# Kernel optimization log

Hardware: AMD Instinct MI355X
Metric: run time of the kernel (lower is better)

The kernel has to match this reference:

```python
import jax, jax.numpy as jnp
import numpy as np

B = 4096          # number of instance groups (images)
C = 81            # num_classes + 1 (fixed by the 81x81 prior_rel buffer)
D_K = 64
MAX_N = 128       # max instances per group


def setup_inputs() -> dict:
    key = jax.random.key(0)
    rng = np.random.default_rng(0)
    ni = rng.integers(1, MAX_N + 1, size=B)
    ni[0] = MAX_N  # pin the max so padded length is deterministic
    num_instances = jnp.asarray(ni, dtype=jnp.int32)
    total = int(ni.sum())
    ks = jax.random.split(key, 10)
    s_in = 1.0 / np.sqrt(C)
    s_dk = 1.0 / np.sqrt(D_K)
    return {
        'x': jax.random.normal(ks[0], (total, C), jnp.float32),
        'num_instances': num_instances,
        'prior_rel': jax.random.normal(ks[1], (C, C), jnp.float32) * s_in,
        'wq': jax.random.normal(ks[2], (C, D_K), jnp.float32) * s_in,
        'bq': jnp.zeros((D_K,), jnp.float32),
        'wk': jax.random.normal(ks[3], (C, D_K), jnp.float32) * s_in,
        'bk': jnp.zeros((D_K,), jnp.float32),
        'wv': jax.random.normal(ks[4], (C, D_K), jnp.float32) * s_in,
        'bv': jnp.zeros((D_K,), jnp.float32),
        'wu': jax.random.normal(ks[5], (D_K, C), jnp.float32) * s_dk,
        'bu': jnp.zeros((C,), jnp.float32),
    }


def reference(x, num_instances, prior_rel, wq, bq, wk, bk, wv, bv, wu, bu):
    # num_instances is static ragged metadata (the torch code keeps it as a
    # Python list), so it is safe to pull concrete ints from it here.
    ni = np.asarray(num_instances)
    Bn = ni.shape[0]
    M = int(ni.max())
    total = x.shape[0]

    counts = jnp.asarray(ni, jnp.int32)                      # [B]
    offsets = jnp.concatenate([jnp.zeros((1,), jnp.int32),
                               jnp.cumsum(counts)[:-1]])      # [B]
    pos = jnp.arange(M, dtype=jnp.int32)                      # [M]
    mask = pos[None, :] < counts[:, None]                     # [B, M] valid slots
    idx = offsets[:, None] + pos[None, :]                     # [B, M] flat gather idx
    idx_safe = jnp.where(mask, idx, 0)

    # pad: split x into ragged groups, zero-pad each to length M
    padded = x[idx_safe] * mask[:, :, None].astype(x.dtype)   # [B, M, C]

    q = padded @ wq + bq                                      # [B, M, d_k]
    k = padded @ wk + bk                                      # [B, M, d_k]
    v = (padded @ prior_rel) @ wv + bv                        # [B, M, d_k]

    scores = jnp.einsum('bmd,bnd->bmn', q, k) / jnp.sqrt(
        jnp.asarray(D_K, x.dtype))                            # [B, M, M]
    # mask padded KEY columns (queries on padded rows are dropped at unpad)
    scores = jnp.where(mask[:, None, :], scores, -jnp.inf)
    probs = jax.nn.softmax(scores, axis=2)
    out = jnp.einsum('bmn,bnd->bmd', probs, v)                # [B, M, d_k]
    out = out @ wu + bu                                       # [B, M, C]

    # unpad: scatter valid rows back to their ragged flat positions
    tgt = jnp.where(mask, idx, total)                         # dump pad rows past end
    flat = jnp.zeros((total + 1, out.shape[-1]), out.dtype)
    flat = flat.at[tgt.reshape(-1)].set(out.reshape(-1, out.shape[-1]))
    return flat[:total]
```

## Files before the change

### kernel.cpp

```cpp
#include <hip/hip_runtime.h>
#include <hip/hip_bf16.h>


typedef __attribute__((ext_vector_type(8))) short short8;
typedef __attribute__((ext_vector_type(4))) float f32x4;
typedef __attribute__((ext_vector_type(4))) short short4v;

constexpr int C  = 81;
constexpr int DK = 64;
constexpr int CP = 96;

constexpr int OFF_K  = 0;
constexpr int OFF_VT = 128 * 64;
constexpr int SMEM_TOT = OFF_VT + 64 * 128;

__device__ inline int kidx(int row, int colu) {
    return OFF_K + row * 64 + (colu ^ ((row & 7) << 3));
}
__device__ inline int vidx(int dim, int colu) {
    return OFF_VT + dim * 128 + (colu ^ ((dim & 15) << 3));
}

__device__ inline ushort f2b(float f) {
    __hip_bfloat16 h = __float2bfloat16(f);
    return *reinterpret_cast<ushort*>(&h);
}
__device__ inline uint pack2bf(float a, float b) {
    return (uint)f2b(a) | ((uint)f2b(b) << 16);
}
__device__ inline uint shflu(uint v, int srcLane) {
    return (uint)__shfl((int)v, srcLane, 64);
}
union U8 { short8 s; uint u[4]; };

__device__ inline short8 cvt8(const f32x4 u0, const f32x4 u1) {
    short8 a;
    #pragma unroll
    for (int e = 0; e < 4; e++) {
        a[e]     = (short)f2b(u0[e]);
        a[e + 4] = (short)f2b(u1[e]);
    }
    return a;
}

__device__ inline void loadx(const float* __restrict__ xr, int quad, f32x4* u) {
    const int c0 = quad * 8;
    __builtin_memcpy(&u[0], xr + c0, 16);
    __builtin_memcpy(&u[1], xr + c0 + 4, 16);
    __builtin_memcpy(&u[2], xr + 32 + c0, 16);
    __builtin_memcpy(&u[3], xr + 32 + c0 + 4, 16);
    u[4] = f32x4{0.f, 0.f, 0.f, 0.f};
    u[5] = f32x4{0.f, 0.f, 0.f, 0.f};
    if (quad < 2) {
        __builtin_memcpy(&u[4], xr + 64 + c0, 16);
        __builtin_memcpy(&u[5], xr + 64 + c0 + 4, 16);
    } else if (quad == 2) {
        u[4][0] = xr[80];
    }
}

#define MFMA16(a, b, c) __builtin_amdgcn_mfma_f32_16x16x32_bf16((a), (b), (c), 0, 0, 0)

__global__ void scan_counts(const int* __restrict__ counts,
                            uint* __restrict__ meta, int n) {
    __shared__ int part[256];
    __shared__ int hist[129];
    __shared__ int start[130];
    const int tid = threadIdx.x;
    for (int i = tid; i < 129; i += 256) hist[i] = 0;
    __syncthreads();
    const int per = (n + 255) >> 8;
    const int base = tid * per;
    int s = 0;
    for (int i = 0; i < per; i++) {
        const int idx = base + i;
        if (idx < n) {
            int c = counts[idx];
            if (c < 0) c = 0; if (c > 128) c = 128;
            s += counts[idx];
            atomicAdd(&hist[c], 1);
        }
    }
    part[tid] = s;
    __syncthreads();
    for (int off = 1; off < 256; off <<= 1) {
        const int v = (tid >= off) ? part[tid - off] : 0;
        __syncthreads();
        part[tid] += v;
        __syncthreads();
    }
    if (tid == 0) {
        start[128] = 0;
        for (int c = 127; c >= 0; c--) start[c] = start[c + 1] + hist[c + 1];
    }
    __syncthreads();
    int run = (tid == 0) ? 0 : part[tid - 1];
    for (int i = 0; i < per; i++) {
        const int idx = base + i;
        if (idx < n) {
            int c = counts[idx];
            int cc = c; if (cc < 0) cc = 0; if (cc > 128) cc = 128;
            const int pos = atomicAdd(&start[cc], 1);
            meta[pos] = (uint)run | ((uint)c << 24);
            run += c;
        }
    }
}

__global__ void prep_weights(const float* __restrict__ prior,
                             const float* __restrict__ wq, const float* __restrict__ wk,
                             const float* __restrict__ wv, const float* __restrict__ wu,
                             ushort* __restrict__ wqT, ushort* __restrict__ wkT,
                             ushort* __restrict__ wvT, ushort* __restrict__ wuT) {
    int idx = blockIdx.x * 256 + threadIdx.x;
    int sec = idx / (DK * CP);
    int i   = idx - sec * (DK * CP);
    if (sec == 0 || sec == 1) {
        int n = i / CP, k = i - (i / CP) * CP;
        const float* w = (sec == 0) ? wq : wk;
        ushort* dst    = (sec == 0) ? wqT : wkT;
        dst[n * CP + k] = (k < C) ? f2b(w[k * DK + n]) : (ushort)0;
    } else if (sec == 2) {
        int n = i / CP, k = i - (i / CP) * CP;
        float s = 0.f;
        if (k < C)
            for (int e = 0; e < C; e++) s = fmaf(prior[k * C + e], wv[e * DK + n], s);
        wvT[n * CP + k] = (k < C) ? f2b(s) : (ushort)0;
    } else {
        int n = i / DK, k = i - (i / DK) * DK;
        wuT[n * DK + k] = (n < C) ? f2b(wu[k * C + n]) : (ushort)0;
    }
}

__launch_bounds__(256, 4)
__global__ void ravnet_mfma(const float* __restrict__ x,
                            const uint* __restrict__ meta,
                            const ushort* __restrict__ wqT, const ushort* __restrict__ wkT,
                            const ushort* __restrict__ wvT, const ushort* __restrict__ wuT,
                            const float* __restrict__ bq, const float* __restrict__ bk,
                            const float* __restrict__ bv, const float* __restrict__ bu,
                            float* __restrict__ out) {
    __shared__ __align__(16) ushort sm[SMEM_TOT];

    const uint mw  = meta[blockIdx.x];
    const int  N   = (int)(mw >> 24);
    const long off = (long)(mw & 0xFFFFFFu);
    const int tid  = threadIdx.x;
    const int lane = tid & 63;
    const int wave = tid >> 6;
    const int quad = lane >> 4;
    const int m16  = lane & 15;
    const int NT8  = (N + 15) >> 4;
    const int NT4  = (N + 31) >> 5;
    const float* xsrc = x + off * C;

    const int srcE = ((quad & 1) << 5) + m16;
    const int srcO = srcE + 16;
    const bool hi  = (quad >> 1) != 0;

    short8 aq[2][2];

    const bool a0 = wave < NT8;
    const bool a1 = (wave + 4) < NT8;
    if (a0) {
        f32x4 xu0[6], xu1[6];
        {
            const int row = wave * 16 + m16;
            const float* xr = xsrc + (long)((row < N) ? row : (N - 1)) * C;
            loadx(xr, quad, xu0);
        }
        if (a1) {
            const int row = (wave + 4) * 16 + m16;
            const float* xr = xsrc + (long)((row < N) ? row : (N - 1)) * C;
            loadx(xr, quad, xu1);
        }
        short8 ax2[2][3];
        ax2[0][0] = cvt8(xu0[0], xu0[1]);
        ax2[0][1] = cvt8(xu0[2], xu0[3]);
        ax2[0][2] = cvt8(xu0[4], xu0[5]);
        if (a1) {
            ax2[1][0] = cvt8(xu1[0], xu1[1]);
            ax2[1][1] = cvt8(xu1[2], xu1[3]);
            ax2[1][2] = cvt8(xu1[4], xu1[5]);
        }
        uint qpk[2][4][2];
        #pragma unroll
        for (int nt = 0; nt < 4; nt++) {
            const ushort* wp = wqT + (nt * 16 + m16) * CP + quad * 8;
            const short8 f0 = *(const short8*)(wp);
            const short8 f1 = *(const short8*)(wp + 32);
            const short8 f2 = *(const short8*)(wp + 64);
            const f32x4 b4 = *(const f32x4*)(bq + nt * 16 + quad * 4);
            {
                f32x4 acc = {0.f, 0.f, 0.f, 0.f};
                acc = MFMA16(f0, ax2[0][0], acc);
                acc = MFMA16(f1, ax2[0][1], acc);
                acc = MFMA16(f2, ax2[0][2], acc);
                qpk[0][nt][0] = pack2bf(acc[0] + b4[0], acc[1] + b4[1]);
                qpk[0][nt][1] = pack2bf(acc[2] + b4[2], acc[3] + b4[3]);
            }
            if (a1) {
                f32x4 acc = {0.f, 0.f, 0.f, 0.f};
                acc = MFMA16(f0, ax2[1][0], acc);
                acc = MFMA16(f1, ax2[1][1], acc);
                acc = MFMA16(f2, ax2[1][2], acc);
                qpk[1][nt][0] = pack2bf(acc[0] + b4[0], acc[1] + b4[1]);
                qpk[1][nt][1] = pack2bf(acc[2] + b4[2], acc[3] + b4[3]);
            }
        }
        #pragma unroll
        for (int t = 0; t < 2; t++) {
            if (t == 0 || a1) {
                #pragma unroll
                for (int ks = 0; ks < 2; ks++) {
                    uint a0v = shflu(qpk[t][2 * ks][0], srcE), b0v = shflu(qpk[t][2 * ks + 1][0], srcE);
                    uint a1v = shflu(qpk[t][2 * ks][1], srcE), b1v = shflu(qpk[t][2 * ks + 1][1], srcE);
                    uint a2v = shflu(qpk[t][2 * ks][0], srcO), b2v = shflu(qpk[t][2 * ks + 1][0], srcO);
                    uint a3v = shflu(qpk[t][2 * ks][1], srcO), b3v = shflu(qpk[t][2 * ks + 1][1], srcO);
                    U8 u;
                    u.u[0] = hi ? b0v : a0v;  u.u[1] = hi ? b1v : a1v;
                    u.u[2] = hi ? b2v : a2v;  u.u[3] = hi ? b3v : a3v;
                    aq[t][ks] = u.s;
                }
            }
        }
        #pragma unroll
        for (int nt = 0; nt < 4; nt++) {
            const ushort* wp = wkT + (nt * 16 + m16) * CP + quad * 8;
            const short8 f0 = *(const short8*)(wp);
            const short8 f1 = *(const short8*)(wp + 32);
            const short8 f2 = *(const short8*)(wp + 64);
            const f32x4 b4 = *(const f32x4*)(bk + nt * 16 + quad * 4);
            {
                f32x4 acc = {0.f, 0.f, 0.f, 0.f};
                acc = MFMA16(f0, ax2[0][0], acc);
                acc = MFMA16(f1, ax2[0][1], acc);
                acc = MFMA16(f2, ax2[0][2], acc);
                short4v pk4;
                #pragma unroll
                for (int r = 0; r < 4; r++) pk4[r] = (short)f2b(acc[r] + b4[r]);
                *(short4v*)(sm + kidx(wave * 16 + m16, nt * 16 + quad * 4)) = pk4;
            }
            if (a1) {
                f32x4 acc = {0.f, 0.f, 0.f, 0.f};
                acc = MFMA16(f0, ax2[1][0], acc);
                acc = MFMA16(f1, ax2[1][1], acc);
                acc = MFMA16(f2, ax2[1][2], acc);
                short4v pk4;
                #pragma unroll
                for (int r = 0; r < 4; r++) pk4[r] = (short)f2b(acc[r] + b4[r]);
                *(short4v*)(sm + kidx((wave + 4) * 16 + m16, nt * 16 + quad * 4)) = pk4;
            }
        }
        #pragma unroll
        for (int nt = 0; nt < 4; nt++) {
            const ushort* wp = wvT + (nt * 16 + m16) * CP + quad * 8;
            const short8 f0 = *(const short8*)(wp);
            const short8 f1 = *(const short8*)(wp + 32);
            const short8 f2 = *(const short8*)(wp + 64);
            const float bb = bv[nt * 16 + m16];
            {
                f32x4 acc = {0.f, 0.f, 0.f, 0.f};
                acc = MFMA16(ax2[0][0], f0, acc);
                acc = MFMA16(ax2[0][1], f1, acc);
                acc = MFMA16(ax2[0][2], f2, acc);
                short4v pk4;
                #pragma unroll
                for (int r = 0; r < 4; r++) pk4[r] = (short)f2b(acc[r] + bb);
                *(short4v*)(sm + vidx(nt * 16 + m16, wave * 16 + quad * 4)) = pk4;
            }
            if (a1) {
                f32x4 acc = {0.f, 0.f, 0.f, 0.f};
                acc = MFMA16(ax2[1][0], f0, acc);
                acc = MFMA16(ax2[1][1], f1, acc);
                acc = MFMA16(ax2[1][2], f2, acc);
                short4v pk4;
                #pragma unroll
                for (int r = 0; r < 4; r++) pk4[r] = (short)f2b(acc[r] + bb);
                *(short4v*)(sm + vidx(nt * 16 + m16, (wave + 4) * 16 + quad * 4)) = pk4;
            }
        }
    }
    if (NT8 & 1) {
        const int R = NT8 * 16;
        const int d = tid >> 2, c4 = (tid & 3) << 2;
        short4v z = {0, 0, 0, 0};
        *(short4v*)(sm + vidx(d, R + c4)) = z;
    }
    __syncthreads();

    constexpr float SCALE = 0.18033688011112042f;
    #pragma unroll
    for (int t = 0; t < 2; t++) {
        const int qt = wave + 4 * t;
        if (qt < NT8) {
            f32x4 sacc[8];
            #pragma unroll
            for (int ct = 0; ct < 8; ct++) {
                if (ct < NT8) {
                    f32x4 a = {0.f, 0.f, 0.f, 0.f};
                    #pragma unroll
                    for (int ks = 0; ks < 2; ks++) {
                        short8 kb = *(const short8*)(sm + kidx(ct * 16 + m16, ks * 32 + quad * 8));
                        a = MFMA16(kb, aq[t][ks], a);
                    }
                    sacc[ct] = a;
                }
            }
            float lr = 0.f;
            #pragma unroll
            for (int ct = 0; ct < 8; ct++) if (ct < NT8) {
                #pragma unroll
                for (int r = 0; r < 4; r++) {
                    const bool valid = (ct * 16 + quad * 4 + r) < N;
                    float p = valid ? __builtin_exp2f(sacc[ct][r] * SCALE) : 0.f;
                    sacc[ct][r] = p;
                    lr += p;
                }
            }
            lr += __shfl_xor(lr, 16, 64);
            lr += __shfl_xor(lr, 32, 64);
            const float linv = 1.f / lr;
            uint pk[8][2];
            #pragma unroll
            for (int ct = 0; ct < 8; ct++) {
                if (ct < NT8) {
                    pk[ct][0] = pack2bf(sacc[ct][0], sacc[ct][1]);
                    pk[ct][1] = pack2bf(sacc[ct][2], sacc[ct][3]);
                } else {
                    pk[ct][0] = 0u; pk[ct][1] = 0u;
                }
            }
            short8 ap[4];
            #pragma unroll
            for (int kt = 0; kt < 4; kt++) {
                if (kt < NT4) {
                    uint a0v = shflu(pk[2 * kt][0], srcE), b0v = shflu(pk[2 * kt + 1][0], srcE);
                    uint a1v = shflu(pk[2 * kt][1], srcE), b1v = shflu(pk[2 * kt + 1][1], srcE);
                    uint a2v = shflu(pk[2 * kt][0], srcO), b2v = shflu(pk[2 * kt + 1][0], srcO);
                    uint a3v = shflu(pk[2 * kt][1], srcO), b3v = shflu(pk[2 * kt + 1][1], srcO);
                    U8 u;
                    u.u[0] = hi ? b0v : a0v;  u.u[1] = hi ? b1v : a1v;
                    u.u[2] = hi ? b2v : a2v;  u.u[3] = hi ? b3v : a3v;
                    ap[kt] = u.s;
                }
            }
            uint opk[4][2];
            #pragma unroll
            for (int ot = 0; ot < 4; ot++) {
                f32x4 oa = {0.f, 0.f, 0.f, 0.f};
                #pragma unroll
                for (int kt = 0; kt < 4; kt++) if (kt < NT4) {
                    short8 vb = *(const short8*)(sm + vidx(ot * 16 + m16, kt * 32 + quad * 8));
                    oa = MFMA16(vb, ap[kt], oa);
                }
                opk[ot][0] = pack2bf(oa[0] * linv, oa[1] * linv);
                opk[ot][1] = pack2bf(oa[2] * linv, oa[3] * linv);
            }
            short8 ao[2];
            #pragma unroll
            for (int ks = 0; ks < 2; ks++) {
                uint a0v = shflu(opk[2 * ks][0], srcE), b0v = shflu(opk[2 * ks + 1][0], srcE);
                uint a1v = shflu(opk[2 * ks][1], srcE), b1v = shflu(opk[2 * ks + 1][1], srcE);
                uint a2v = shflu(opk[2 * ks][0], srcO), b2v = shflu(opk[2 * ks + 1][0], srcO);
                uint a3v = shflu(opk[2 * ks][1], srcO), b3v = shflu(opk[2 * ks + 1][1], srcO);
                U8 u;
                u.u[0] = hi ? b0v : a0v;  u.u[1] = hi ? b1v : a1v;
                u.u[2] = hi ? b2v : a2v;  u.u[3] = hi ? b3v : a3v;
                ao[ks] = u.s;
            }
            const int xrow = qt * 16 + m16;
            float* orow = out + (off + xrow) * C;
            #pragma unroll
            for (int ct = 0; ct < 6; ct++) {
                f32x4 acc = {0.f, 0.f, 0.f, 0.f};
                #pragma unroll
                for (int ks = 0; ks < 2; ks++) {
                    short8 wb = *(const short8*)(wuT + (ct * 16 + m16) * DK + ks * 32 + quad * 8);
                    acc = MFMA16(wb, ao[ks], acc);
                }
                const int e0 = ct * 16 + quad * 4;
                if (xrow < N) {
                    if (e0 + 3 < C) {
                        const f32x4 b4 = *(const f32x4*)(bu + e0);
                        acc[0] += b4[0]; acc[1] += b4[1];
                        acc[2] += b4[2]; acc[3] += b4[3];
                        __builtin_memcpy(orow + e0, &acc, 16);
                    } else if (e0 == 80) {
                        orow[80] = acc[0] + bu[80];
                    }
                }
            }
        }
    }
}

extern "C" void kernel_launch(void* const* d_in, const int* in_sizes, int n_in,
                              void* d_out, int out_size, void* d_ws, size_t ws_size,
                              hipStream_t stream) {
    const float* x      = (const float*)d_in[0];
    const int*   counts = (const int*)  d_in[1];
    const float* prior  = (const float*)d_in[2];
    const float* wq     = (const float*)d_in[3];
    const float* bq     = (const float*)d_in[4];
    const float* wk     = (const float*)d_in[5];
    const float* bk     = (const float*)d_in[6];
    const float* wv     = (const float*)d_in[7];
    const float* bv     = (const float*)d_in[8];
    const float* wu     = (const float*)d_in[9];
    const float* bu     = (const float*)d_in[10];
    float* out = (float*)d_out;

    const int B = in_sizes[1];

    uint*   meta = (uint*)d_ws;
    ushort* wqT = (ushort*)((char*)d_ws + (((size_t)B * sizeof(uint) + 255) & ~(size_t)255));
    ushort* wkT = wqT + DK * CP;
    ushort* wvT = wkT + DK * CP;
    ushort* wuT = wvT + DK * CP;

    scan_counts<<<1, 256, 0, stream>>>(counts, meta, B);
    prep_weights<<<(4 * DK * CP + 255) / 256, 256, 0, stream>>>(
        prior, wq, wk, wv, wu, wqT, wkT, wvT, wuT);
    ravnet_mfma<<<B, 256, 0, stream>>>(x, meta,
                                       wqT, wkT, wvT, wuT,
                                       bq, bk, bv, bu, out);
}
```

Baseline: 243.5 us.

## Process both query tiles of a wave jointly to share K/V LDS loads

The attention phase now handles a wave's two query tiles together through a templated lambda (dual or single path). Each K and V fragment read from shared memory, and each Wu weight load, feeds two MFMAs instead of being reloaded per tile, and the independent MFMA chains can interleave. The x row loads for both tiles are also issued up front to overlap their global memory latency. In exchange the dual path roughly doubles live accumulator and packing registers, which could lower occupancy or cause spills, and two code paths are compiled.

```diff
diff --git a/kernel.cpp b/kernel.cpp
--- a/kernel.cpp
+++ b/kernel.cpp
@@ -32,6 +32,12 @@
     return (uint)__shfl((int)v, srcLane, 64);
 }
 union U8 { short8 s; uint u[4]; };
+
+__device__ __forceinline__ f32x4 ld4u(const float* p) {
+    f32x4 v;
+    __builtin_memcpy(&v, p, 16);
+    return v;
+}
 
 __device__ inline short8 cvt8(const f32x4 u0, const f32x4 u1) {
     short8 a;
@@ -43,23 +49,20 @@
     return a;
 }
 
-__device__ inline void loadx(const float* __restrict__ xr, int quad, f32x4* u) {
-    const int c0 = quad * 8;
-    __builtin_memcpy(&u[0], xr + c0, 16);
-    __builtin_memcpy(&u[1], xr + c0 + 4, 16);
-    __builtin_memcpy(&u[2], xr + 32 + c0, 16);
-    __builtin_memcpy(&u[3], xr + 32 + c0 + 4, 16);
-    u[4] = f32x4{0.f, 0.f, 0.f, 0.f};
-    u[5] = f32x4{0.f, 0.f, 0.f, 0.f};
-    if (quad < 2) {
-        __builtin_memcpy(&u[4], xr + 64 + c0, 16);
-        __builtin_memcpy(&u[5], xr + 64 + c0 + 4, 16);
-    } else if (quad == 2) {
-        u[4][0] = xr[80];
-    }
-}
-
 #define MFMA16(a, b, c) __builtin_amdgcn_mfma_f32_16x16x32_bf16((a), (b), (c), 0, 0, 0)
+
+#define XPOSE(dst, pA0, pA1, pB0, pB1) do {                                   \
+    uint _a0 = shflu(pA0, srcE), _b0 = shflu(pB0, srcE);                      \
+    uint _a1 = shflu(pA1, srcE), _b1 = shflu(pB1, srcE);                      \
+    uint _a2 = shflu(pA0, srcO), _b2 = shflu(pB0, srcO);                      \
+    uint _a3 = shflu(pA1, srcO), _b3 = shflu(pB1, srcO);                      \
+    U8 _u;                                                                    \
+    _u.u[0] = hi ? _b0 : _a0;  _u.u[1] = hi ? _b1 : _a1;                      \
+    _u.u[2] = hi ? _b2 : _a2;  _u.u[3] = hi ? _b3 : _a3;                      \
+    dst = _u.s; } while (0)
+
+struct BT { static constexpr bool value = true;  };
+struct BF { static constexpr bool value = false; };
 
 __global__ void scan_counts(const int* __restrict__ counts,
                             uint* __restrict__ meta, int n) {
@@ -163,25 +166,32 @@
     const bool a0 = wave < NT8;
     const bool a1 = (wave + 4) < NT8;
     if (a0) {
-        f32x4 xu0[6], xu1[6];
-        {
-            const int row = wave * 16 + m16;
-            const float* xr = xsrc + (long)((row < N) ? row : (N - 1)) * C;
-            loadx(xr, quad, xu0);
-        }
+        const int c0 = quad * 8;
+        const int row0 = wave * 16 + m16;
+        const int row1 = (wave + 4) * 16 + m16;
+        const float* xr0 = xsrc + (long)((row0 < N) ? row0 : (N - 1)) * C;
+        const float* xr1 = a1 ? (xsrc + (long)((row1 < N) ? row1 : (N - 1)) * C) : xr0;
+        f32x4 p00 = ld4u(xr0 + c0),      p01 = ld4u(xr0 + c0 + 4);
+        f32x4 p02 = ld4u(xr0 + 32 + c0), p03 = ld4u(xr0 + 32 + c0 + 4);
+        f32x4 p10 = ld4u(xr1 + c0),      p11 = ld4u(xr1 + c0 + 4);
+        f32x4 p12 = ld4u(xr1 + 32 + c0), p13 = ld4u(xr1 + 32 + c0 + 4);
+        f32x4 p04 = {0.f, 0.f, 0.f, 0.f}, p05 = {0.f, 0.f, 0.f, 0.f};
+        f32x4 p14 = {0.f, 0.f, 0.f, 0.f}, p15 = {0.f, 0.f, 0.f, 0.f};
+        if (quad < 2) {
+            p04 = ld4u(xr0 + 64 + c0); p05 = ld4u(xr0 + 64 + c0 + 4);
+            p14 = ld4u(xr1 + 64 + c0); p15 = ld4u(xr1 + 64 + c0 + 4);
+        } else if (quad == 2) {
+            p04[0] = xr0[80];
+            p14[0] = xr1[80];
+        }
+        short8 ax2[2][3];
+        ax2[0][0] = cvt8(p00, p01);
+        ax2[0][1] = cvt8(p02, p03);
+        ax2[0][2] = cvt8(p04, p05);
         if (a1) {
-            const int row = (wave + 4) * 16 + m16;
-            const float* xr = xsrc + (long)((row < N) ? row : (N - 1)) * C;
-            loadx(xr, quad, xu1);
-        }
-        short8 ax2[2][3];
-        ax2[0][0] = cvt8(xu0[0], xu0[1]);
-        ax2[0][1] = cvt8(xu0[2], xu0[3]);
-        ax2[0][2] = cvt8(xu0[4], xu0[5]);
-        if (a1) {
-            ax2[1][0] = cvt8(xu1[0], xu1[1]);
-            ax2[1][1] = cvt8(xu1[2], xu1[3]);
-            ax2[1][2] = cvt8(xu1[4], xu1[5]);
+            ax2[1][0] = cvt8(p10, p11);
+            ax2[1][1] = cvt8(p12, p13);
+            ax2[1][2] = cvt8(p14, p15);
         }
         uint qpk[2][4][2];
         #pragma unroll
@@ -209,20 +219,14 @@
             }
         }
         #pragma unroll
-        for (int t = 0; t < 2; t++) {
-            if (t == 0 || a1) {
-                #pragma unroll
-                for (int ks = 0; ks < 2; ks++) {
-                    uint a0v = shflu(qpk[t][2 * ks][0], srcE), b0v = shflu(qpk[t][2 * ks + 1][0], srcE);
-                    uint a1v = shflu(qpk[t][2 * ks][1], srcE), b1v = shflu(qpk[t][2 * ks + 1][1], srcE);
-                    uint a2v = shflu(qpk[t][2 * ks][0], srcO), b2v = shflu(qpk[t][2 * ks + 1][0], srcO);
-                    uint a3v = shflu(qpk[t][2 * ks][1], srcO), b3v = shflu(qpk[t][2 * ks + 1][1], srcO);
-                    U8 u;
-                    u.u[0] = hi ? b0v : a0v;  u.u[1] = hi ? b1v : a1v;
-                    u.u[2] = hi ? b2v : a2v;  u.u[3] = hi ? b3v : a3v;
-                    aq[t][ks] = u.s;
-                }
-            }
+        for (int ks = 0; ks < 2; ks++)
+            XPOSE(aq[0][ks], qpk[0][2 * ks][0], qpk[0][2 * ks][1],
+                             qpk[0][2 * ks + 1][0], qpk[0][2 * ks + 1][1]);
+        if (a1) {
+            #pragma unroll
+            for (int ks = 0; ks < 2; ks++)
+                XPOSE(aq[1][ks], qpk[1][2 * ks][0], qpk[1][2 * ks][1],
+                                 qpk[1][2 * ks + 1][0], qpk[1][2 * ks + 1][1]);
         }
         #pragma unroll
         for (int nt = 0; nt < 4; nt++) {
@@ -290,108 +294,131 @@
     __syncthreads();
 
     constexpr float SCALE = 0.18033688011112042f;
-    #pragma unroll
-    for (int t = 0; t < 2; t++) {
-        const int qt = wave + 4 * t;
-        if (qt < NT8) {
-            f32x4 sacc[8];
-            #pragma unroll
-            for (int ct = 0; ct < 8; ct++) {
-                if (ct < NT8) {
-                    f32x4 a = {0.f, 0.f, 0.f, 0.f};
-                    #pragma unroll
-                    for (int ks = 0; ks < 2; ks++) {
-                        short8 kb = *(const short8*)(sm + kidx(ct * 16 + m16, ks * 32 + quad * 8));
-                        a = MFMA16(kb, aq[t][ks], a);
-                    }
-                    sacc[ct] = a;
-                }
-            }
-            float lr = 0.f;
-            #pragma unroll
-            for (int ct = 0; ct < 8; ct++) if (ct < NT8) {
-                #pragma unroll
-                for (int r = 0; r < 4; r++) {
-                    const bool valid = (ct * 16 + quad * 4 + r) < N;
-                    float p = valid ? __builtin_exp2f(sacc[ct][r] * SCALE) : 0.f;
-                    sacc[ct][r] = p;
-                    lr += p;
-                }
-            }
-            lr += __shfl_xor(lr, 16, 64);
-            lr += __shfl_xor(lr, 32, 64);
-            const float linv = 1.f / lr;
-            uint pk[8][2];
-            #pragma unroll
-            for (int ct = 0; ct < 8; ct++) {
-                if (ct < NT8) {
-                    pk[ct][0] = pack2bf(sacc[ct][0], sacc[ct][1]);
-                    pk[ct][1] = pack2bf(sacc[ct][2], sacc[ct][3]);
-                } else {
-                    pk[ct][0] = 0u; pk[ct][1] = 0u;
-                }
-            }
-            short8 ap[4];
-            #pragma unroll
-            for (int kt = 0; kt < 4; kt++) {
-                if (kt < NT4) {
-                    uint a0v = shflu(pk[2 * kt][0], srcE), b0v = shflu(pk[2 * kt + 1][0], srcE);
-                    uint a1v = shflu(pk[2 * kt][1], srcE), b1v = shflu(pk[2 * kt + 1][1], srcE);
-                    uint a2v = shflu(pk[2 * kt][0], srcO), b2v = shflu(pk[2 * kt + 1][0], srcO);
-                    uint a3v = shflu(pk[2 * kt][1], srcO), b3v = shflu(pk[2 * kt + 1][1], srcO);
-                    U8 u;
-                    u.u[0] = hi ? b0v : a0v;  u.u[1] = hi ? b1v : a1v;
-                    u.u[2] = hi ? b2v : a2v;  u.u[3] = hi ? b3v : a3v;
-                    ap[kt] = u.s;
-                }
-            }
-            uint opk[4][2];
-            #pragma unroll
-            for (int ot = 0; ot < 4; ot++) {
-                f32x4 oa = {0.f, 0.f, 0.f, 0.f};
-                #pragma unroll
-                for (int kt = 0; kt < 4; kt++) if (kt < NT4) {
-                    short8 vb = *(const short8*)(sm + vidx(ot * 16 + m16, kt * 32 + quad * 8));
-                    oa = MFMA16(vb, ap[kt], oa);
-                }
-                opk[ot][0] = pack2bf(oa[0] * linv, oa[1] * linv);
-                opk[ot][1] = pack2bf(oa[2] * linv, oa[3] * linv);
-            }
-            short8 ao[2];
+    auto phase2 = [&](auto dualc) {
+        constexpr bool DUAL = decltype(dualc)::value;
+        f32x4 s0[8], s1[8];
+        #pragma unroll
+        for (int ct = 0; ct < 8; ct++) if (ct < NT8) {
+            f32x4 A0 = {0.f, 0.f, 0.f, 0.f};
+            f32x4 A1 = {0.f, 0.f, 0.f, 0.f};
             #pragma unroll
             for (int ks = 0; ks < 2; ks++) {
-                uint a0v = shflu(opk[2 * ks][0], srcE), b0v = shflu(opk[2 * ks + 1][0], srcE);
-                uint a1v = shflu(opk[2 * ks][1], srcE), b1v = shflu(opk[2 * ks + 1][1], srcE);
-                uint a2v = shflu(opk[2 * ks][0], srcO), b2v = shflu(opk[2 * ks + 1][0], srcO);
-                uint a3v = shflu(opk[2 * ks][1], srcO), b3v = shflu(opk[2 * ks + 1][1], srcO);
-                U8 u;
-                u.u[0] = hi ? b0v : a0v;  u.u[1] = hi ? b1v : a1v;
-                u.u[2] = hi ? b2v : a2v;  u.u[3] = hi ? b3v : a3v;
-                ao[ks] = u.s;
-            }
-            const int xrow = qt * 16 + m16;
-            float* orow = out + (off + xrow) * C;
+                short8 kb = *(const short8*)(sm + kidx(ct * 16 + m16, ks * 32 + quad * 8));
+                A0 = MFMA16(kb, aq[0][ks], A0);
+                if (DUAL) A1 = MFMA16(kb, aq[1][ks], A1);
+            }
+            s0[ct] = A0;
+            if (DUAL) s1[ct] = A1;
+        }
+        float lr0 = 0.f, lr1 = 0.f;
+        #pragma unroll
+        for (int ct = 0; ct < 8; ct++) if (ct < NT8) {
             #pragma unroll
-            for (int ct = 0; ct < 6; ct++) {
-                f32x4 acc = {0.f, 0.f, 0.f, 0.f};
-                #pragma unroll
-                for (int ks = 0; ks < 2; ks++) {
-                    short8 wb = *(const short8*)(wuT + (ct * 16 + m16) * DK + ks * 32 + quad * 8);
-                    acc = MFMA16(wb, ao[ks], acc);
+            for (int r = 0; r < 4; r++) {
+                const bool valid = (ct * 16 + quad * 4 + r) < N;
+                float p0 = valid ? __builtin_exp2f(s0[ct][r] * SCALE) : 0.f;
+                s0[ct][r] = p0; lr0 += p0;
+                if (DUAL) {
+                    float p1 = valid ? __builtin_exp2f(s1[ct][r] * SCALE) : 0.f;
+                    s1[ct][r] = p1; lr1 += p1;
                 }
-                const int e0 = ct * 16 + quad * 4;
-                if (xrow < N) {
-                    if (e0 + 3 < C) {
-                        const f32x4 b4 = *(const f32x4*)(bu + e0);
-                        acc[0] += b4[0]; acc[1] += b4[1];
-                        acc[2] += b4[2]; acc[3] += b4[3];
-                        __builtin_memcpy(orow + e0, &acc, 16);
-                    } else if (e0 == 80) {
-                        orow[80] = acc[0] + bu[80];
-                    }
+            }
+        }
+        lr0 += __shfl_xor(lr0, 16, 64);
+        lr0 += __shfl_xor(lr0, 32, 64);
+        const float linv0 = 1.f / lr0;
+        float linv1 = 0.f;
+        if (DUAL) {
+            lr1 += __shfl_xor(lr1, 16, 64);
+            lr1 += __shfl_xor(lr1, 32, 64);
+            linv1 = 1.f / lr1;
+        }
+        uint pk0[8][2], pk1[8][2];
+        #pragma unroll
+        for (int ct = 0; ct < 8; ct++) {
+            if (ct < NT8) {
+                pk0[ct][0] = pack2bf(s0[ct][0], s0[ct][1]);
+                pk0[ct][1] = pack2bf(s0[ct][2], s0[ct][3]);
+                if (DUAL) {
+                    pk1[ct][0] = pack2bf(s1[ct][0], s1[ct][1]);
+                    pk1[ct][1] = pack2bf(s1[ct][2], s1[ct][3]);
                 }
-            }
-        }
+            } else {
+                pk0[ct][0] = 0u; pk0[ct][1] = 0u;
+                if (DUAL) { pk1[ct][0] = 0u; pk1[ct][1] = 0u; }
+            }
+        }
+        short8 ap0[4], ap1[4];
+        #pragma unroll
+        for (int kt = 0; kt < 4; kt++) if (kt < NT4) {
+            XPOSE(ap0[kt], pk0[2 * kt][0], pk0[2 * kt][1],
+                           pk0[2 * kt + 1][0], pk0[2 * kt + 1][1]);
+            if (DUAL)
+                XPOSE(ap1[kt], pk1[2 * kt][0], pk1[2 * kt][1],
+                               pk1[2 * kt + 1][0], pk1[2 * kt + 1][1]);
+        }
+        uint opk0[4][2], opk1[4][2];
+        #pragma unroll
+        for (int ot = 0; ot < 4; ot++) {
+            f32x4 o0 = {0.f, 0.f, 0.f, 0.f};
+            f32x4 o1 = {0.f, 0.f, 0.f, 0.f};
+            #pragma unroll
+            for (int kt = 0; kt < 4; kt++) if (kt < NT4) {
+                short8 vb = *(const short8*)(sm + vidx(ot * 16 + m16, kt * 32 + quad * 8));
+                o0 = MFMA16(vb, ap0[kt], o0);
+                if (DUAL) o1 = MFMA16(vb, ap1[kt], o1);
+            }
+            opk0[ot][0] = pack2bf(o0[0] * linv0, o0[1] * linv0);
+            opk0[ot][1] = pack2bf(o0[2] * linv0, o0[3] * linv0);
+            if (DUAL) {
+                opk1[ot][0] = pack2bf(o1[0] * linv1, o1[1] * linv1);
+                opk1[ot][1] = pack2bf(o1[2] * linv1, o1[3] * linv1);
+            }
+        }
+        short8 ao0[2], ao1[2];
+        #pragma unroll
+        for (int ks = 0; ks < 2; ks++) {
+            XPOSE(ao0[ks], opk0[2 * ks][0], opk0[2 * ks][1],
+                           opk0[2 * ks + 1][0], opk0[2 * ks + 1][1]);
+            if (DUAL)
+                XPOSE(ao1[ks], opk1[2 * ks][0], opk1[2 * ks][1],
+                               opk1[2 * ks + 1][0], opk1[2 * ks + 1][1]);
+        }
+        const int xrow0 = wave * 16 + m16;
+        const int xrow1 = (wave + 4) * 16 + m16;
+        float* orow0 = out + (off + xrow0) * C;
+        float* orow1 = out + (off + xrow1) * C;
+        #pragma unroll
+        for (int ct = 0; ct < 6; ct++) {
+            const ushort* wp = wuT + (ct * 16 + m16) * DK + quad * 8;
+            const short8 wb0 = *(const short8*)(wp);
+            const short8 wb1 = *(const short8*)(wp + 32);
+            f32x4 A0 = {0.f, 0.f, 0.f, 0.f};
+            f32x4 A1 = {0.f, 0.f, 0.f, 0.f};
+            A0 = MFMA16(wb0, ao0[0], A0);
+            A0 = MFMA16(wb1, ao0[1], A0);
+            if (DUAL) {
+                A1 = MFMA16(wb0, ao1[0], A1);
+                A1 = MFMA16(wb1, ao1[1], A1);
+            }
+            const int e0 = ct * 16 + quad * 4;
+            if (e0 + 3 < C) {
+                const f32x4 b4 = *(const f32x4*)(bu + e0);
+                A0[0] += b4[0]; A0[1] += b4[1]; A0[2] += b4[2]; A0[3] += b4[3];
+                if (xrow0 < N) __builtin_memcpy(orow0 + e0, &A0, 16);
+                if (DUAL) {
+                    A1[0] += b4[0]; A1[1] += b4[1]; A1[2] += b4[2]; A1[3] += b4[3];
+                    if (xrow1 < N) __builtin_memcpy(orow1 + e0, &A1, 16);
+                }
+            } else if (e0 == 80) {
+                if (xrow0 < N) orow0[80] = A0[0] + bu[80];
+                if (DUAL && xrow1 < N) orow1[80] = A1[0] + bu[80];
+            }
+        }
+    };
+    if (a0) {
+        if (a1) phase2(BT{});
+        else    phase2(BF{});
     }
 }
 
```

New measurement: 245.9 us. Within noise of the previous version (+1.0%).
